# Optimization experiments

Hardware: AMD Instinct MI355X
Metric: run time of the kernel (lower is better)

The kernel has to match this reference:

```python
import jax, jax.numpy as jnp
import numpy as np
from jax import lax

DN = ('NCHW', 'OIHW', 'NCHW')

def conv(x, w, b, stride):
    y = lax.conv_general_dilated(x, w, window_strides=(stride, stride),
                                 padding='VALID', dimension_numbers=DN)
    return y + b[None, :, None, None]

def setup_inputs() -> dict:
    key = jax.random.key(0)
    ks = jax.random.split(key, 7)
    B = 4096
    def he(k, shape, fan_in):
        return jax.random.normal(k, shape, jnp.float32) * np.sqrt(2.0 / fan_in)
    return {
        'x':  jax.random.normal(ks[0], (B, 3, 48, 64), jnp.float32),
        'w1': he(ks[1], (32, 3, 8, 8), 3 * 8 * 8),
        'b1': jnp.zeros((32,), jnp.float32),
        'w2': he(ks[2], (64, 32, 3, 3), 32 * 3 * 3),
        'b2': jnp.zeros((64,), jnp.float32),
        'w3': he(ks[3], (64, 64, 3, 3), 64 * 3 * 3),
        'b3': jnp.zeros((64,), jnp.float32),
        'w4': he(ks[4], (512, 960), 960),
        'b4': jnp.zeros((512,), jnp.float32),
        'w5': he(ks[5], (2, 512), 512),
        'b5': jnp.zeros((2,), jnp.float32),
    }

def reference(x, w1, b1, w2, b2, w3, b3, w4, b4, w5, b5):
    # conv1 (k8 s4): [B,3,48,64] -> [B,32,11,15]
    x1 = conv(x, w1, b1, 4)
    # side reduction (torch code does this on CPU with python loops):
    # sum over batch and channel dims of pre-ReLU activation, divided by 32
    ave1 = jnp.sum(x1, axis=(0, 1)) / 32.0          # [11,15]
    x2 = jax.nn.relu(x1)
    # conv2 (k3 s2): -> [B,64,5,7]
    x3 = conv(x2, w2, b2, 2)
    ave2 = jnp.sum(x3, axis=(0, 1)) / 64.0          # [5,7]
    x4 = jax.nn.relu(x3)
    # conv3 (k3 s1): -> [B,64,3,5]
    x5 = conv(x4, w3, b3, 1)
    ave3 = jnp.sum(x5, axis=(0, 1)) / 64.0          # [3,5]
    x6 = jax.nn.relu(x5)
    # fc head: flatten (C,H,W order, matching torch) -> 960 -> 512 -> 2
    h = x6.reshape(x6.shape[0], -1)                 # [B,960]
    h = jax.nn.relu(h @ w4.T + b4)
    out = h @ w5.T + b5                             # [B,2]
    return out, ave1, ave2, ave3
```

## Files before the change

### kernel.cpp

```cpp
#include <hip/hip_runtime.h>
#include <hip/hip_bf16.h>

#define BATCH 4096

typedef __attribute__((ext_vector_type(8))) short short8;
typedef __attribute__((ext_vector_type(4))) short short4_t;
typedef __attribute__((ext_vector_type(4))) float f32x4;

#define MFMA_BF16 __builtin_amdgcn_mfma_f32_16x16x32_bf16

#define WWAIT() asm volatile("s_waitcnt lgkmcnt(0)" ::: "memory")

__device__ __forceinline__ float frelu(float v) { return v > 0.f ? v : 0.f; }
__device__ __forceinline__ unsigned short f2bf(float f) {
    return __builtin_bit_cast(unsigned short, __float2bfloat16(f));
}

__global__ __launch_bounds__(256) void prep_kernel(const float* __restrict__ w1, const float* __restrict__ w2,
                                                   const float* __restrict__ w3, const float* __restrict__ w4,
                                                   const float* __restrict__ b5,
                                                   unsigned short* __restrict__ w1p, unsigned short* __restrict__ w2p,
                                                   unsigned short* __restrict__ w3p, unsigned short* __restrict__ w4p,
                                                   float* __restrict__ out) {
    int idx = blockIdx.x * 256 + threadIdx.x;
    if (idx < 6144) {
        w1p[idx] = f2bf(w1[idx]);
    } else if (idx < 24576) {
        int j = idx - 6144;
        int oc = j / 288, k = j % 288;
        int khw = k / 32, ic = k % 32;
        w2p[j] = f2bf(w2[oc * 288 + ic * 9 + khw]);
    } else if (idx < 61440) {
        int j = idx - 24576;
        int oc = j / 576, k = j % 576;
        int khw = k / 64, ic = k % 64;
        w3p[j] = f2bf(w3[oc * 576 + ic * 9 + khw]);
    } else if (idx < 552960) {
        int j = idx - 61440;
        int n = j / 960, k = j % 960;
        int pos = k / 64, oc = k % 64;
        w4p[j] = f2bf(w4[n * 960 + oc * 15 + pos]);
    } else if (idx < 561152) {
        int j = idx - 552960;
        out[j] = b5[j & 1];
    } else if (idx < 561367) {
        out[8192 + (idx - 561152)] = 0.f;
    }
}

__global__ __launch_bounds__(256, 2) void fused_convs(const float* __restrict__ x,
                                                      const unsigned short* __restrict__ w1p, const float* __restrict__ b1,
                                                      const unsigned short* __restrict__ w2p, const float* __restrict__ b2,
                                                      const unsigned short* __restrict__ w3p, const float* __restrict__ b3,
                                                      unsigned short* __restrict__ x6, float* __restrict__ redbuf) {
    __shared__ __align__(16) unsigned short S[4][9792];
    const int tid = threadIdx.x;
    const int wave = tid >> 6, lane = tid & 63;
    const int col = lane & 15, quad = lane >> 4;
    const int img = blockIdx.x * 4 + wave;

    unsigned short* ub  = S[wave];
    unsigned short* x2l = ub;
    unsigned short* x4l = ub + 5952;
    float* redrow = redbuf + (size_t)img * 216;

    {
        const float4* xs = (const float4*)(x + (size_t)img * 9216);
        #pragma unroll
        for (int b = 0; b < 3; ++b) {
            float4 t[12];
            #pragma unroll
            for (int i = 0; i < 12; ++i) t[i] = xs[lane + (b * 12 + i) * 64];
            #pragma unroll
            for (int i = 0; i < 12; ++i) {
                const int idx = lane + (b * 12 + i) * 64;
                const int r = idx >> 4, cf = (idx & 15) * 4;
                short4_t s;
                s[0] = (short)f2bf(t[i].x); s[1] = (short)f2bf(t[i].y);
                s[2] = (short)f2bf(t[i].z); s[3] = (short)f2bf(t[i].w);
                *(short4_t*)(ub + r * 68 + cf) = s;
            }
        }
    }
    WWAIT();

    short8 Bf1[2][6];
    #pragma unroll
    for (int nt = 0; nt < 2; ++nt) {
        const unsigned short* wb = w1p + (size_t)(nt * 16 + col) * 192 + quad * 8;
        #pragma unroll
        for (int c = 0; c < 6; ++c) Bf1[nt][c] = *(const short8*)(wb + c * 32);
    }
    f32x4 c1a[11][2] = {};
    #pragma unroll
    for (int t = 0; t < 11; ++t) {
        const int posA = t * 16 + col;
        const int pm = posA < 165 ? posA : 164;
        const int oh = pm / 15, ow = pm % 15;
        #pragma unroll
        for (int c = 0; c < 6; ++c) {
            const int ic = c >> 1;
            const int kh = (c & 1) * 4 + quad;
            const unsigned short* ap = ub + (ic * 48 + oh * 4 + kh) * 68 + ow * 4;
            short8 af;
            *(short4_t*)&af       = *(const short4_t*)ap;
            *((short4_t*)&af + 1) = *(const short4_t*)(ap + 4);
            c1a[t][0] = MFMA_BF16(af, Bf1[0][c], c1a[t][0], 0, 0, 0);
            c1a[t][1] = MFMA_BF16(af, Bf1[1][c], c1a[t][1], 0, 0, 0);
        }
    }
    WWAIT();

    {
        const float bias0 = b1[col], bias1 = b1[col + 16];
        #pragma unroll
        for (int t = 0; t < 11; ++t) {
            #pragma unroll
            for (int r = 0; r < 4; ++r) {
                const int pr = t * 16 + quad * 4 + r;
                float v0 = c1a[t][0][r] + bias0;
                float v1 = c1a[t][1][r] + bias1;
                float s = v0 + v1;
                s += __shfl_xor(s, 1); s += __shfl_xor(s, 2);
                s += __shfl_xor(s, 4); s += __shfl_xor(s, 8);
                if (pr < 165) {
                    x2l[pr * 36 + col]      = f2bf(frelu(v0));
                    x2l[pr * 36 + col + 16] = f2bf(frelu(v1));
                    if (col == 0) redrow[pr] = s;
                }
            }
        }
    }
    WWAIT();

    {
        int aoff[3];
        #pragma unroll
        for (int mt = 0; mt < 3; ++mt) {
            int p = mt * 16 + col; p = p < 35 ? p : 34;
            aoff[mt] = ((p / 7) * 30 + (p % 7) * 2) * 36 + quad * 8;
        }
        f32x4 a2[3][4] = {};
        #pragma unroll
        for (int c = 0; c < 9; ++c) {
            const int koff = ((c / 3) * 15 + (c % 3)) * 36;
            short8 A[3];
            #pragma unroll
            for (int mt = 0; mt < 3; ++mt) {
                const unsigned short* ap = x2l + aoff[mt] + koff;
                *(short4_t*)&A[mt]       = *(const short4_t*)ap;
                *((short4_t*)&A[mt] + 1) = *(const short4_t*)(ap + 4);
            }
            #pragma unroll
            for (int nt = 0; nt < 4; ++nt) {
                short8 Bc = *(const short8*)(w2p + (size_t)(nt * 16 + col) * 288 + c * 32 + quad * 8);
                #pragma unroll
                for (int mt = 0; mt < 3; ++mt)
                    a2[mt][nt] = MFMA_BF16(A[mt], Bc, a2[mt][nt], 0, 0, 0);
            }
        }
        float bv2[4];
        #pragma unroll
        for (int nt = 0; nt < 4; ++nt) bv2[nt] = b2[nt * 16 + col];
        #pragma unroll
        for (int mt = 0; mt < 3; ++mt) {
            #pragma unroll
            for (int r = 0; r < 4; ++r) {
                const int pr = mt * 16 + quad * 4 + r;
                if (pr < 35) {
                    float s = 0.f;
                    #pragma unroll
                    for (int nt = 0; nt < 4; ++nt) {
                        float v = a2[mt][nt][r] + bv2[nt];
                        s += v;
                        x4l[pr * 72 + nt * 16 + col] = f2bf(frelu(v));
                    }
                    s += __shfl_xor(s, 1); s += __shfl_xor(s, 2);
                    s += __shfl_xor(s, 4); s += __shfl_xor(s, 8);
                    if (col == 0) redrow[165 + pr] = s;
                }
            }
        }
    }
    WWAIT();

    {
        int p = col < 15 ? col : 14;
        const int abase = ((p / 5) * 7 + (p % 5)) * 72;
        f32x4 a3[4] = {};
        #pragma unroll
        for (int cc = 0; cc < 9; ++cc) {
            const unsigned short* bp = x4l + abase + ((cc / 3) * 7 + (cc % 3)) * 72 + quad * 8;
            short8 af0 = *(const short8*)bp;
            short8 af1 = *(const short8*)(bp + 32);
            #pragma unroll
            for (int nt = 0; nt < 4; ++nt) {
                const unsigned short* wb = w3p + (size_t)(nt * 16 + col) * 576 + quad * 8;
                short8 B0 = *(const short8*)(wb + (2 * cc) * 32);
                short8 B1 = *(const short8*)(wb + (2 * cc + 1) * 32);
                a3[nt] = MFMA_BF16(af0, B0, a3[nt], 0, 0, 0);
                a3[nt] = MFMA_BF16(af1, B1, a3[nt], 0, 0, 0);
            }
        }
        float bv3[4];
        #pragma unroll
        for (int nt = 0; nt < 4; ++nt) bv3[nt] = b3[nt * 16 + col];
        unsigned short* xout = x6 + (size_t)img * 960;
        #pragma unroll
        for (int r = 0; r < 4; ++r) {
            const int pr = quad * 4 + r;
            if (pr < 15) {
                float s = 0.f;
                #pragma unroll
                for (int nt = 0; nt < 4; ++nt) {
                    float v = a3[nt][r] + bv3[nt];
                    s += v;
                    xout[pr * 64 + nt * 16 + col] = f2bf(frelu(v));
                }
                s += __shfl_xor(s, 1); s += __shfl_xor(s, 2);
                s += __shfl_xor(s, 4); s += __shfl_xor(s, 8);
                if (col == 0) redrow[200 + pr] = s;
            }
        }
    }
}

__global__ __launch_bounds__(256) void reduce_aves(const float* __restrict__ redbuf, float* __restrict__ out) {
    const int row = blockIdx.x;
    float s = 0.f;
    for (int i = threadIdx.x; i < 4096; i += 256) s += redbuf[(size_t)i * 216 + row];
    s += __shfl_down(s, 32); s += __shfl_down(s, 16); s += __shfl_down(s, 8);
    s += __shfl_down(s, 4);  s += __shfl_down(s, 2);  s += __shfl_down(s, 1);
    __shared__ float wsum[4];
    if ((threadIdx.x & 63) == 0) wsum[threadIdx.x >> 6] = s;
    __syncthreads();
    if (threadIdx.x == 0)
        out[8192 + row] = (wsum[0] + wsum[1] + wsum[2] + wsum[3]) * (row < 165 ? 0.03125f : 0.015625f);
}

__global__ __launch_bounds__(256) void fc45_mfma(const unsigned short* __restrict__ x6,
                                                 const unsigned short* __restrict__ w4p, const float* __restrict__ b4,
                                                 const float* __restrict__ w5, float* __restrict__ out) {
    __shared__ float outl[32][2];
    const int tid = threadIdx.x;
    const int wave = tid >> 6, lane = tid & 63;
    const int col = lane & 15, quad = lane >> 4;
    if (tid < 64) outl[tid >> 1][tid & 1] = 0.f;
    const int m0 = blockIdx.x * 32;
    const int oc = blockIdx.y * 64 + wave * 16 + col;

    const unsigned short* brow  = w4p + (size_t)oc * 960 + quad * 8;
    const unsigned short* arow0 = x6 + (size_t)(m0 + col) * 960 + quad * 8;
    const unsigned short* arow1 = arow0 + 16 * 960;
    f32x4 acc0 = {}, acc1 = {};
    __syncthreads();
    #pragma unroll 6
    for (int c = 0; c < 30; ++c) {
        short8 Bf = *(const short8*)(brow + c * 32);
        short8 a0 = *(const short8*)(arow0 + c * 32);
        short8 a1 = *(const short8*)(arow1 + c * 32);
        acc0 = MFMA_BF16(a0, Bf, acc0, 0, 0, 0);
        acc1 = MFMA_BF16(a1, Bf, acc1, 0, 0, 0);
    }
    const float bb = b4[oc], u0 = w5[oc], u1 = w5[512 + oc];
    #pragma unroll
    for (int mi = 0; mi < 2; ++mi) {
        const f32x4 acc = mi ? acc1 : acc0;
        #pragma unroll
        for (int r = 0; r < 4; ++r) {
            float h = frelu(acc[r] + bb);
            float l0 = h * u0, l1 = h * u1;
            l0 += __shfl_xor(l0, 1); l0 += __shfl_xor(l0, 2); l0 += __shfl_xor(l0, 4); l0 += __shfl_xor(l0, 8);
            l1 += __shfl_xor(l1, 1); l1 += __shfl_xor(l1, 2); l1 += __shfl_xor(l1, 4); l1 += __shfl_xor(l1, 8);
            if (col == 0) {
                atomicAdd(&outl[mi * 16 + quad * 4 + r][0], l0);
                atomicAdd(&outl[mi * 16 + quad * 4 + r][1], l1);
            }
        }
    }
    __syncthreads();
    if (tid < 64) atomicAdd(&out[(m0 + (tid >> 1)) * 2 + (tid & 1)], outl[tid >> 1][tid & 1]);
}

extern "C" void kernel_launch(void* const* d_in, const int* in_sizes, int n_in,
                              void* d_out, int out_size, void* d_ws, size_t ws_size,
                              hipStream_t stream) {
    const float* x  = (const float*)d_in[0];
    const float* w1 = (const float*)d_in[1];
    const float* b1 = (const float*)d_in[2];
    const float* w2 = (const float*)d_in[3];
    const float* b2 = (const float*)d_in[4];
    const float* w3 = (const float*)d_in[5];
    const float* b3 = (const float*)d_in[6];
    const float* w4 = (const float*)d_in[7];
    const float* b4 = (const float*)d_in[8];
    const float* w5 = (const float*)d_in[9];
    const float* b5 = (const float*)d_in[10];
    float* out = (float*)d_out;

    unsigned short* ws = (unsigned short*)d_ws;
    unsigned short* x6  = ws;
    unsigned short* w1p = ws + 3932160;
    unsigned short* w2p = ws + 3938304;
    unsigned short* w3p = ws + 3956736;
    unsigned short* w4p = ws + 3993600;
    float* redbuf = (float*)((char*)d_ws + 8970240);

    prep_kernel<<<2193, 256, 0, stream>>>(w1, w2, w3, w4, b5, w1p, w2p, w3p, w4p, out);
    fused_convs<<<1024, 256, 0, stream>>>(x, w1p, b1, w2p, b2, w3p, b3, x6, redbuf);
    reduce_aves<<<215, 256, 0, stream>>>(redbuf, out);
    fc45_mfma<<<dim3(128, 8), 256, 0, stream>>>(x6, w4p, b4, w5, out);
}
```

Measured before the change: 341.0 us.

## Split each image's conv pipeline across two waves with block barriers

Each image is now handled by a pair of waves instead of one. The pair splits the input load, the conv1 M-tiles and the conv2/conv3 output channels, and synchronises through s_barrier between stages. Per-wave register pressure drops (conv1 accumulators halve), the launch-bounds occupancy hint is removed, and the grid doubles. In exchange it adds block-wide barriers, duplicated A-fragment loads, and a doubled side-reduction buffer that reduce_aves must now sum over twice as many rows.

```diff
diff --git a/kernel.cpp b/kernel.cpp
--- a/kernel.cpp
+++ b/kernel.cpp
@@ -9,7 +9,7 @@
 
 #define MFMA_BF16 __builtin_amdgcn_mfma_f32_16x16x32_bf16
 
-#define WWAIT() asm volatile("s_waitcnt lgkmcnt(0)" ::: "memory")
+#define LBAR() asm volatile("s_waitcnt lgkmcnt(0)\n\ts_barrier" ::: "memory")
 
 __device__ __forceinline__ float frelu(float v) { return v > 0.f ? v : 0.f; }
 __device__ __forceinline__ unsigned short f2bf(float f) {
@@ -48,32 +48,33 @@
     }
 }
 
-__global__ __launch_bounds__(256, 2) void fused_convs(const float* __restrict__ x,
-                                                      const unsigned short* __restrict__ w1p, const float* __restrict__ b1,
-                                                      const unsigned short* __restrict__ w2p, const float* __restrict__ b2,
-                                                      const unsigned short* __restrict__ w3p, const float* __restrict__ b3,
-                                                      unsigned short* __restrict__ x6, float* __restrict__ redbuf) {
-    __shared__ __align__(16) unsigned short S[4][9792];
+__global__ __launch_bounds__(256) void fused_convs(const float* __restrict__ x,
+                                                   const unsigned short* __restrict__ w1p, const float* __restrict__ b1,
+                                                   const unsigned short* __restrict__ w2p, const float* __restrict__ b2,
+                                                   const unsigned short* __restrict__ w3p, const float* __restrict__ b3,
+                                                   unsigned short* __restrict__ x6, float* __restrict__ redbuf) {
+    __shared__ __align__(16) unsigned short S[2][9792];
     const int tid = threadIdx.x;
     const int wave = tid >> 6, lane = tid & 63;
     const int col = lane & 15, quad = lane >> 4;
-    const int img = blockIdx.x * 4 + wave;
-
-    unsigned short* ub  = S[wave];
+    const int p = wave & 1;
+    const int img = blockIdx.x * 2 + (wave >> 1);
+
+    unsigned short* ub  = S[wave >> 1];
     unsigned short* x2l = ub;
     unsigned short* x4l = ub + 5952;
-    float* redrow = redbuf + (size_t)img * 216;
+    float* vrow = redbuf + ((size_t)img * 2 + p) * 216;
 
     {
         const float4* xs = (const float4*)(x + (size_t)img * 9216);
         #pragma unroll
-        for (int b = 0; b < 3; ++b) {
-            float4 t[12];
-            #pragma unroll
-            for (int i = 0; i < 12; ++i) t[i] = xs[lane + (b * 12 + i) * 64];
-            #pragma unroll
-            for (int i = 0; i < 12; ++i) {
-                const int idx = lane + (b * 12 + i) * 64;
+        for (int b = 0; b < 2; ++b) {
+            float4 t[9];
+            #pragma unroll
+            for (int i = 0; i < 9; ++i) t[i] = xs[(b * 9 + i) * 128 + p * 64 + lane];
+            #pragma unroll
+            for (int i = 0; i < 9; ++i) {
+                const int idx = (b * 9 + i) * 128 + p * 64 + lane;
                 const int r = idx >> 4, cf = (idx & 15) * 4;
                 short4_t s;
                 s[0] = (short)f2bf(t[i].x); s[1] = (short)f2bf(t[i].y);
@@ -82,7 +83,7 @@
             }
         }
     }
-    WWAIT();
+    LBAR();
 
     short8 Bf1[2][6];
     #pragma unroll
@@ -91,9 +92,11 @@
         #pragma unroll
         for (int c = 0; c < 6; ++c) Bf1[nt][c] = *(const short8*)(wb + c * 32);
     }
-    f32x4 c1a[11][2] = {};
+    f32x4 c1a[6][2] = {};
     #pragma unroll
-    for (int t = 0; t < 11; ++t) {
+    for (int ti = 0; ti < 6; ++ti) {
+        const int t = ti * 2 + p;
+        if (t >= 11) break;
         const int posA = t * 16 + col;
         const int pm = posA < 165 ? posA : 164;
         const int oh = pm / 15, ow = pm % 15;
@@ -105,42 +108,46 @@
             short8 af;
             *(short4_t*)&af       = *(const short4_t*)ap;
             *((short4_t*)&af + 1) = *(const short4_t*)(ap + 4);
-            c1a[t][0] = MFMA_BF16(af, Bf1[0][c], c1a[t][0], 0, 0, 0);
-            c1a[t][1] = MFMA_BF16(af, Bf1[1][c], c1a[t][1], 0, 0, 0);
-        }
-    }
-    WWAIT();
+            c1a[ti][0] = MFMA_BF16(af, Bf1[0][c], c1a[ti][0], 0, 0, 0);
+            c1a[ti][1] = MFMA_BF16(af, Bf1[1][c], c1a[ti][1], 0, 0, 0);
+        }
+    }
+    LBAR();
 
     {
         const float bias0 = b1[col], bias1 = b1[col + 16];
         #pragma unroll
-        for (int t = 0; t < 11; ++t) {
+        for (int ti = 0; ti < 6; ++ti) {
+            const int t = ti * 2 + p;
+            if (t >= 11) break;
             #pragma unroll
             for (int r = 0; r < 4; ++r) {
                 const int pr = t * 16 + quad * 4 + r;
-                float v0 = c1a[t][0][r] + bias0;
-                float v1 = c1a[t][1][r] + bias1;
+                float v0 = c1a[ti][0][r] + bias0;
+                float v1 = c1a[ti][1][r] + bias1;
                 float s = v0 + v1;
                 s += __shfl_xor(s, 1); s += __shfl_xor(s, 2);
                 s += __shfl_xor(s, 4); s += __shfl_xor(s, 8);
                 if (pr < 165) {
                     x2l[pr * 36 + col]      = f2bf(frelu(v0));
                     x2l[pr * 36 + col + 16] = f2bf(frelu(v1));
-                    if (col == 0) redrow[pr] = s;
+                    if (col == 0) vrow[pr] = s;
                 }
             }
         }
-    }
-    WWAIT();
+        for (int i = lane; i < 165; i += 64)
+            if (((i >> 4) & 1) != p) vrow[i] = 0.f;
+    }
+    LBAR();
 
     {
         int aoff[3];
         #pragma unroll
         for (int mt = 0; mt < 3; ++mt) {
-            int p = mt * 16 + col; p = p < 35 ? p : 34;
-            aoff[mt] = ((p / 7) * 30 + (p % 7) * 2) * 36 + quad * 8;
-        }
-        f32x4 a2[3][4] = {};
+            int pp = mt * 16 + col; pp = pp < 35 ? pp : 34;
+            aoff[mt] = ((pp / 7) * 30 + (pp % 7) * 2) * 36 + quad * 8;
+        }
+        f32x4 a2[3][2] = {};
         #pragma unroll
         for (int c = 0; c < 9; ++c) {
             const int koff = ((c / 3) * 15 + (c % 3)) * 36;
@@ -152,16 +159,16 @@
                 *((short4_t*)&A[mt] + 1) = *(const short4_t*)(ap + 4);
             }
             #pragma unroll
-            for (int nt = 0; nt < 4; ++nt) {
-                short8 Bc = *(const short8*)(w2p + (size_t)(nt * 16 + col) * 288 + c * 32 + quad * 8);
+            for (int n = 0; n < 2; ++n) {
+                short8 Bc = *(const short8*)(w2p + (size_t)(p * 32 + n * 16 + col) * 288 + c * 32 + quad * 8);
                 #pragma unroll
                 for (int mt = 0; mt < 3; ++mt)
-                    a2[mt][nt] = MFMA_BF16(A[mt], Bc, a2[mt][nt], 0, 0, 0);
-            }
-        }
-        float bv2[4];
-        #pragma unroll
-        for (int nt = 0; nt < 4; ++nt) bv2[nt] = b2[nt * 16 + col];
+                    a2[mt][n] = MFMA_BF16(A[mt], Bc, a2[mt][n], 0, 0, 0);
+            }
+        }
+        float bv2[2];
+        #pragma unroll
+        for (int n = 0; n < 2; ++n) bv2[n] = b2[p * 32 + n * 16 + col];
         #pragma unroll
         for (int mt = 0; mt < 3; ++mt) {
             #pragma unroll
@@ -170,41 +177,41 @@
                 if (pr < 35) {
                     float s = 0.f;
                     #pragma unroll
-                    for (int nt = 0; nt < 4; ++nt) {
-                        float v = a2[mt][nt][r] + bv2[nt];
+                    for (int n = 0; n < 2; ++n) {
+                        float v = a2[mt][n][r] + bv2[n];
                         s += v;
-                        x4l[pr * 72 + nt * 16 + col] = f2bf(frelu(v));
+                        x4l[pr * 72 + p * 32 + n * 16 + col] = f2bf(frelu(v));
                     }
                     s += __shfl_xor(s, 1); s += __shfl_xor(s, 2);
                     s += __shfl_xor(s, 4); s += __shfl_xor(s, 8);
-                    if (col == 0) redrow[165 + pr] = s;
+                    if (col == 0) vrow[165 + pr] = s;
                 }
             }
         }
     }
-    WWAIT();
+    LBAR();
 
     {
-        int p = col < 15 ? col : 14;
-        const int abase = ((p / 5) * 7 + (p % 5)) * 72;
-        f32x4 a3[4] = {};
+        int pp = col < 15 ? col : 14;
+        const int abase = ((pp / 5) * 7 + (pp % 5)) * 72;
+        f32x4 a3[2] = {};
         #pragma unroll
         for (int cc = 0; cc < 9; ++cc) {
             const unsigned short* bp = x4l + abase + ((cc / 3) * 7 + (cc % 3)) * 72 + quad * 8;
             short8 af0 = *(const short8*)bp;
             short8 af1 = *(const short8*)(bp + 32);
             #pragma unroll
-            for (int nt = 0; nt < 4; ++nt) {
-                const unsigned short* wb = w3p + (size_t)(nt * 16 + col) * 576 + quad * 8;
+            for (int n = 0; n < 2; ++n) {
+                const unsigned short* wb = w3p + (size_t)(p * 32 + n * 16 + col) * 576 + quad * 8;
                 short8 B0 = *(const short8*)(wb + (2 * cc) * 32);
                 short8 B1 = *(const short8*)(wb + (2 * cc + 1) * 32);
-                a3[nt] = MFMA_BF16(af0, B0, a3[nt], 0, 0, 0);
-                a3[nt] = MFMA_BF16(af1, B1, a3[nt], 0, 0, 0);
-            }
-        }
-        float bv3[4];
-        #pragma unroll
-        for (int nt = 0; nt < 4; ++nt) bv3[nt] = b3[nt * 16 + col];
+                a3[n] = MFMA_BF16(af0, B0, a3[n], 0, 0, 0);
+                a3[n] = MFMA_BF16(af1, B1, a3[n], 0, 0, 0);
+            }
+        }
+        float bv3[2];
+        #pragma unroll
+        for (int n = 0; n < 2; ++n) bv3[n] = b3[p * 32 + n * 16 + col];
         unsigned short* xout = x6 + (size_t)img * 960;
         #pragma unroll
         for (int r = 0; r < 4; ++r) {
@@ -212,14 +219,14 @@
             if (pr < 15) {
                 float s = 0.f;
                 #pragma unroll
-                for (int nt = 0; nt < 4; ++nt) {
-                    float v = a3[nt][r] + bv3[nt];
+                for (int n = 0; n < 2; ++n) {
+                    float v = a3[n][r] + bv3[n];
                     s += v;
-                    xout[pr * 64 + nt * 16 + col] = f2bf(frelu(v));
+                    xout[pr * 64 + p * 32 + n * 16 + col] = f2bf(frelu(v));
                 }
                 s += __shfl_xor(s, 1); s += __shfl_xor(s, 2);
                 s += __shfl_xor(s, 4); s += __shfl_xor(s, 8);
-                if (col == 0) redrow[200 + pr] = s;
+                if (col == 0) vrow[200 + pr] = s;
             }
         }
     }
@@ -228,7 +235,7 @@
 __global__ __launch_bounds__(256) void reduce_aves(const float* __restrict__ redbuf, float* __restrict__ out) {
     const int row = blockIdx.x;
     float s = 0.f;
-    for (int i = threadIdx.x; i < 4096; i += 256) s += redbuf[(size_t)i * 216 + row];
+    for (int i = threadIdx.x; i < 8192; i += 256) s += redbuf[(size_t)i * 216 + row];
     s += __shfl_down(s, 32); s += __shfl_down(s, 16); s += __shfl_down(s, 8);
     s += __shfl_down(s, 4);  s += __shfl_down(s, 2);  s += __shfl_down(s, 1);
     __shared__ float wsum[4];
@@ -307,7 +314,7 @@
     float* redbuf = (float*)((char*)d_ws + 8970240);
 
     prep_kernel<<<2193, 256, 0, stream>>>(w1, w2, w3, w4, b5, w1p, w2p, w3p, w4p, out);
-    fused_convs<<<1024, 256, 0, stream>>>(x, w1p, b1, w2p, b2, w3p, b3, x6, redbuf);
+    fused_convs<<<2048, 256, 0, stream>>>(x, w1p, b1, w2p, b2, w3p, b3, x6, redbuf);
     reduce_aves<<<215, 256, 0, stream>>>(redbuf, out);
     fc45_mfma<<<dim3(128, 8), 256, 0, stream>>>(x6, w4p, b4, w5, out);
 }
```

Result: faster. 328.2 us (-3.7%).
